# Optimization experiments

Measured on AMD Instinct MI355X. Metric: run time of the kernel, lower is better.

Reference implementation:

```python
import jax, jax.numpy as jnp
import numpy as np

NUM_CLASSES = 1000
TEMPERATURE = 0.1
B, B_OOD, D = 4096, 4096, 512


def _l2norm(x):
    return x / jnp.linalg.norm(x, axis=-1, keepdims=True)


def setup_inputs() -> dict:
    key = jax.random.key(0)
    k1, k2, k3, k4, k5 = jax.random.split(key, 5)
    return {
        "centers1": _l2norm(jax.random.normal(k1, (NUM_CLASSES, D), dtype=jnp.float32)),
        "features": _l2norm(jax.random.normal(k2, (B, D), dtype=jnp.float32)),
        "targets": jax.random.randint(k3, (B,), 0, NUM_CLASSES, dtype=jnp.int64 if jax.config.jax_enable_x64 else jnp.int32),
        "features_ood": _l2norm(jax.random.normal(k4, (B_OOD, D), dtype=jnp.float32)),
        "pseudo_target_ood": jax.random.randint(k5, (B_OOD,), 0, NUM_CLASSES, dtype=jnp.int64 if jax.config.jax_enable_x64 else jnp.int32),
    }


def reference(centers1, features, targets, features_ood, pseudo_target_ood):
    C = centers1.shape[0]
    b = features.shape[0]
    bo = features_ood.shape[0]
    n = b + C + bo  # total anchors: batch + class centers + ood

    centers_lbl = jnp.arange(C, dtype=targets.dtype)
    ood_lbl = jnp.full((bo,), C, dtype=targets.dtype)  # ood gets label == num_classes
    targets_all = jnp.concatenate([targets, centers_lbl, ood_lbl])              # [N]
    targets_all_class = jnp.concatenate([targets, centers_lbl, pseudo_target_ood])  # [N]

    # per-class count over all N labels (pseudo labels for ood)
    batch_cls_count = jnp.zeros((C,), dtype=jnp.float32).at[targets_all_class].add(1.0)

    # positive mask: same label as anchor, excluding self (diagonal for j < B)
    mask = (targets_all[:b, None] == targets_all[None, :]).astype(jnp.float32)  # [B,N]
    logits_mask = 1.0 - (jnp.arange(n)[None, :] == jnp.arange(b)[:, None]).astype(jnp.float32)
    mask = mask * logits_mask

    features_all = jnp.concatenate([features, centers1, features_ood], axis=0)  # [N,D]
    logits = jnp.matmul(features, features_all.T) / TEMPERATURE                 # [B,N]
    logits = logits - jax.lax.stop_gradient(jnp.max(logits, axis=1, keepdims=True))

    exp_logits = jnp.exp(logits) * logits_mask
    # class-balanced per-instance weight (count of the column's class, minus positive mask)
    per_ins_weight = batch_cls_count[targets_all_class][None, :] - mask         # [B,N]
    exp_logits_sum = jnp.sum(exp_logits / per_ins_weight, axis=1, keepdims=True)
    log_prob = logits - jnp.log(exp_logits_sum)

    mean_log_prob_pos = jnp.sum(mask * log_prob, axis=1) / jnp.sum(mask, axis=1)
    loss = -jnp.mean(mean_log_prob_pos)
    return loss
```

## Files before the change

### kernel.cpp

```cpp
#include <hip/hip_runtime.h>
#include <hip/hip_bf16.h>
#include <stdint.h>

#define NUM_C 1000
#define NB    4096
#define NO    4096
#define NCOL  9192
#define NPAD  9216
#define DK    512
#define BM    128
#define BN    256
#define BK    32
#define INV_T 10.0f

typedef __attribute__((ext_vector_type(8))) short short8;
typedef __attribute__((ext_vector_type(4))) float f32x4;

#define OFF_FALL 0u
#define OFF_CNT  9437184u
#define OFF_CNTT 9441280u
#define OFF_S    9445376u
#define OFF_P    9461760u
#define ZERO_BYTES 40960u

__device__ __forceinline__ void async16(const void* g, void* l) {
  __builtin_amdgcn_global_load_lds((const __attribute__((address_space(1))) void*)g,
                                   (__attribute__((address_space(3))) void*)l,
                                   16, 0, 0);
}

__device__ __forceinline__ ushort f2bf_rne(float f) {
  uint32_t u = __builtin_bit_cast(uint32_t, f);
  u += 0x7FFFu + ((u >> 16) & 1u);
  return (ushort)(u >> 16);
}

__global__ __launch_bounds__(256) void prep_k(const float* __restrict__ centers,
                                              const float* __restrict__ feats,
                                              const float* __restrict__ ood,
                                              const int* __restrict__ targets,
                                              const int* __restrict__ pseudo,
                                              ushort* __restrict__ fall,
                                              unsigned* __restrict__ cnt,
                                              unsigned* __restrict__ cntT) {
  int idx = blockIdx.x * 256 + threadIdx.x;
  int row = idx >> 6;
  int ck  = (idx & 63) * 8;
  ushort h[8];
  const float* src = nullptr;
  if (row < NB)              src = feats   + (size_t)row * DK + ck;
  else if (row < NB + NUM_C) src = centers + (size_t)(row - NB) * DK + ck;
  else if (row < NCOL)       src = ood     + (size_t)(row - NB - NUM_C) * DK + ck;
  if (src) {
    float4 v0 = *(const float4*)(src);
    float4 v1 = *(const float4*)(src + 4);
    h[0] = f2bf_rne(v0.x); h[1] = f2bf_rne(v0.y); h[2] = f2bf_rne(v0.z); h[3] = f2bf_rne(v0.w);
    h[4] = f2bf_rne(v1.x); h[5] = f2bf_rne(v1.y); h[6] = f2bf_rne(v1.z); h[7] = f2bf_rne(v1.w);
  } else {
    for (int i = 0; i < 8; i++) h[i] = 0;
  }
  *(uint4*)(fall + (size_t)row * DK + ck) = *(uint4*)h;

  if (blockIdx.x < 16) {
    int i = blockIdx.x * 256 + threadIdx.x;
    int t = targets[i];
    atomicAdd(&cnt[t], 1u);
    atomicAdd(&cntT[t], 1u);
    atomicAdd(&cnt[pseudo[i]], 1u);
  }
}

__global__ __launch_bounds__(256, 2) void gemm_fused(const ushort* __restrict__ fall,
                                                     const int* __restrict__ targets,
                                                     const int* __restrict__ pseudo,
                                                     const unsigned* __restrict__ cnt,
                                                     float* __restrict__ Sacc,
                                                     float* __restrict__ Pacc) {
  __shared__ ushort As[BM * BK];
  __shared__ ushort Bs[BN * BK];
  __shared__ int    sLbl[BN];
  __shared__ float  sRw0[BN];
  __shared__ float  sRw1[BN];
  __shared__ int    sTgt[BM];

  const int tid   = threadIdx.x;
  const int nTile = blockIdx.x;
  const int mTile = blockIdx.y;
  const int lane  = tid & 63;
  const int wv    = tid >> 6;
  const int wm    = wv >> 1;
  const int wn    = wv & 1;
  const int q     = lane >> 4;
  const int cIdx  = lane & 15;

  {
    int j = nTile * BN + tid;
    int lbl, tac;
    if (j >= NCOL)         { lbl = -1; tac = -1; }
    else if (j < NB)       { tac = targets[j]; lbl = tac; }
    else if (j < NB+NUM_C) { tac = j - NB;     lbl = tac; }
    else                   { tac = pseudo[j - NB - NUM_C]; lbl = NUM_C; }
    sLbl[tid] = lbl;
    if (tac >= 0) {
      float w = (float)(cnt[tac] + 1u);
      sRw0[tid] = 1.0f / w;
      sRw1[tid] = 1.0f / (w - 1.0f);
    } else {
      sRw0[tid] = 0.f;
      sRw1[tid] = 0.f;
    }
    if (tid < BM) sTgt[tid] = targets[mTile * BM + tid];
  }

  f32x4 acc[4][8];
#pragma unroll
  for (int mi = 0; mi < 4; mi++)
#pragma unroll
    for (int ni = 0; ni < 8; ni++)
      acc[mi][ni] = (f32x4){0.f, 0.f, 0.f, 0.f};

  const int aRow0 = mTile * BM;
  const int bRow0 = nTile * BN;
  const int sRow  = tid >> 2;
  const int sKo   = (tid & 3) * 8;

  for (int kt = 0; kt < DK; kt += BK) {
    __syncthreads();
    async16(fall + (size_t)(aRow0 + sRow)       * DK + kt + sKo, &As[sRow * BK + sKo]);
    async16(fall + (size_t)(aRow0 + 64 + sRow)  * DK + kt + sKo, &As[(64 + sRow) * BK + sKo]);
    async16(fall + (size_t)(bRow0 + sRow)       * DK + kt + sKo, &Bs[sRow * BK + sKo]);
    async16(fall + (size_t)(bRow0 + 64 + sRow)  * DK + kt + sKo, &Bs[(64 + sRow) * BK + sKo]);
    async16(fall + (size_t)(bRow0 + 128 + sRow) * DK + kt + sKo, &Bs[(128 + sRow) * BK + sKo]);
    async16(fall + (size_t)(bRow0 + 192 + sRow) * DK + kt + sKo, &Bs[(192 + sRow) * BK + sKo]);
    __syncthreads();

    short8 af[4], bfr[8];
#pragma unroll
    for (int mi = 0; mi < 4; mi++)
      af[mi] = *(const short8*)&As[(wm * 64 + mi * 16 + cIdx) * BK + q * 8];
#pragma unroll
    for (int ni = 0; ni < 8; ni++)
      bfr[ni] = *(const short8*)&Bs[(wn * 128 + ni * 16 + cIdx) * BK + q * 8];
#pragma unroll
    for (int mi = 0; mi < 4; mi++)
#pragma unroll
      for (int ni = 0; ni < 8; ni++)
        acc[mi][ni] = __builtin_amdgcn_mfma_f32_16x16x32_bf16(af[mi], bfr[ni], acc[mi][ni], 0, 0, 0);
  }

  float vS[16], vP[16];
#pragma unroll
  for (int s = 0; s < 16; s++) { vS[s] = 0.f; vP[s] = 0.f; }

#pragma unroll
  for (int ni = 0; ni < 8; ni++) {
    int jloc = wn * 128 + ni * 16 + cIdx;
    int j    = nTile * BN + jloc;
    int lblj = sLbl[jloc];
    float rw0 = sRw0[jloc], rw1 = sRw1[jloc];
#pragma unroll
    for (int mi = 0; mi < 4; mi++) {
      f32x4 a = acc[mi][ni];
#pragma unroll
      for (int r = 0; r < 4; r++) {
        int iloc = wm * 64 + mi * 16 + q * 4 + r;
        int i    = mTile * BM + iloc;
        int ti   = sTgt[iloc];
        float l  = a[r] * INV_T;
        bool diag = (j == i);
        bool pos  = (lblj == ti) && !diag;
        float rw  = diag ? 0.0f : (pos ? rw1 : rw0);
        float e   = __expf(l - 10.0f) * rw;
        vS[mi * 4 + r] += e;
        vP[mi * 4 + r] += pos ? l : 0.0f;
      }
    }
  }

#define RED_STEP(m, s, h)                                        \
  {                                                              \
    float sendS = (cIdx & (m)) ? vS[(s)] : vS[(s) + (h)];        \
    float sendP = (cIdx & (m)) ? vP[(s)] : vP[(s) + (h)];        \
    float rS = __shfl_xor(sendS, (m), 64);                       \
    float rP = __shfl_xor(sendP, (m), 64);                       \
    vS[(s)] = ((cIdx & (m)) ? vS[(s) + (h)] : vS[(s)]) + rS;     \
    vP[(s)] = ((cIdx & (m)) ? vP[(s) + (h)] : vP[(s)]) + rP;     \
  }
  RED_STEP(8, 0, 8) RED_STEP(8, 1, 8) RED_STEP(8, 2, 8) RED_STEP(8, 3, 8)
  RED_STEP(8, 4, 8) RED_STEP(8, 5, 8) RED_STEP(8, 6, 8) RED_STEP(8, 7, 8)
  RED_STEP(4, 0, 4) RED_STEP(4, 1, 4) RED_STEP(4, 2, 4) RED_STEP(4, 3, 4)
  RED_STEP(2, 0, 2) RED_STEP(2, 1, 2)
  RED_STEP(1, 0, 1)
#undef RED_STEP

  {
    int rowLoc = wm * 64 + (cIdx >> 2) * 16 + q * 4 + (cIdx & 3);
    int i = mTile * BM + rowLoc;
    atomicAdd(&Sacc[i], vS[0]);
    atomicAdd(&Pacc[i], vP[0]);
  }
}

__global__ __launch_bounds__(256) void finalize_k(const float* __restrict__ S,
                                                  const float* __restrict__ P,
                                                  const int* __restrict__ targets,
                                                  const unsigned* __restrict__ cntT,
                                                  float* __restrict__ out) {
  __shared__ float red[4];
  int tid = threadIdx.x;
  float local = 0.f;
  for (int i = tid; i < NB; i += 256) {
    float npos = (float)cntT[targets[i]];
    local += P[i] / npos - INV_T - __logf(S[i]);
  }
  for (int m = 1; m < 64; m <<= 1) local += __shfl_xor(local, m, 64);
  if ((tid & 63) == 0) red[tid >> 6] = local;
  __syncthreads();
  if (tid == 0) {
    float t = red[0] + red[1] + red[2] + red[3];
    out[0] = -t / (float)NB;
  }
}

extern "C" void kernel_launch(void* const* d_in, const int* in_sizes, int n_in,
                              void* d_out, int out_size, void* d_ws, size_t ws_size,
                              hipStream_t stream) {
  const float* centers = (const float*)d_in[0];
  const float* feats   = (const float*)d_in[1];
  const int*   targets = (const int*)d_in[2];
  const float* ood     = (const float*)d_in[3];
  const int*   pseudo  = (const int*)d_in[4];

  char* ws = (char*)d_ws;
  ushort*   fall = (ushort*)(ws + OFF_FALL);
  unsigned* cnt  = (unsigned*)(ws + OFF_CNT);
  unsigned* cntT = (unsigned*)(ws + OFF_CNTT);
  float*    Sacc = (float*)(ws + OFF_S);
  float*    Pacc = (float*)(ws + OFF_P);

  hipMemsetAsync(ws + OFF_CNT, 0, ZERO_BYTES, stream);
  prep_k<<<dim3((NPAD * 64) / 256), 256, 0, stream>>>(centers, feats, ood, targets, pseudo,
                                                      fall, cnt, cntT);
  gemm_fused<<<dim3(NPAD / BN, NB / BM), 256, 0, stream>>>(fall, targets, pseudo, cnt, Sacc, Pacc);
  finalize_k<<<1, 256, 0, stream>>>(Sacc, Pacc, targets, cntT, (float*)d_out);
}
```

Baseline: 144.0 us.

## Switch GEMM operands to FP8 e4m3 and replace memset with per-block histograms

Features are converted to FP8 e4m3 instead of bf16, and the GEMM uses the 16x16x32 fp8 MFMA, with a swizzled LDS layout and half as many async loads per K step. Class counts are built in shared-memory histograms per block and written as partials that the GEMM and finalize kernels sum. This drops the memset launch; the S/P accumulators are now zeroed inside prep_k. FP8 operands lower the precision of the logits, and since the temperature scales them by ten, rounding error in the exponentials grows and may hurt accuracy.

```diff
diff --git a/kernel.cpp b/kernel.cpp
--- a/kernel.cpp
+++ b/kernel.cpp
@@ -1,27 +1,23 @@
 #include <hip/hip_runtime.h>
-#include <hip/hip_bf16.h>
 #include <stdint.h>
 
 #define NUM_C 1000
 #define NB    4096
-#define NO    4096
 #define NCOL  9192
 #define NPAD  9216
 #define DK    512
 #define BM    128
 #define BN    256
-#define BK    32
+#define BKB   32
 #define INV_T 10.0f
 
-typedef __attribute__((ext_vector_type(8))) short short8;
 typedef __attribute__((ext_vector_type(4))) float f32x4;
 
-#define OFF_FALL 0u
-#define OFF_CNT  9437184u
-#define OFF_CNTT 9441280u
-#define OFF_S    9445376u
-#define OFF_P    9461760u
-#define ZERO_BYTES 40960u
+#define OFF_FALL  0u
+#define OFF_CNTP  4718592u
+#define OFF_CNTTP 4784128u
+#define OFF_S     4849664u
+#define OFF_P     4866048u
 
 __device__ __forceinline__ void async16(const void* g, void* l) {
   __builtin_amdgcn_global_load_lds((const __attribute__((address_space(1))) void*)g,
@@ -29,10 +25,32 @@
                                    16, 0, 0);
 }
 
-__device__ __forceinline__ ushort f2bf_rne(float f) {
-  uint32_t u = __builtin_bit_cast(uint32_t, f);
-  u += 0x7FFFu + ((u >> 16) & 1u);
-  return (ushort)(u >> 16);
+__device__ __forceinline__ unsigned sw_e4m3(float x) {
+  float ax = fabsf(x);
+  unsigned s = (__float_as_uint(x) >> 24) & 0x80u;
+  if (ax < 0.015625f) {
+    int n = (int)rintf(ax * 512.0f);
+    if (n >= 8) return s | 0x08u;
+    return s | (unsigned)n;
+  }
+  if (ax >= 448.0f) return s | 0x7Eu;
+  unsigned u = __float_as_uint(ax);
+  int ee = (int)(u >> 23) - 127;
+  float scale = __uint_as_float((unsigned)(3 - ee + 127) << 23);
+  int qv = (int)rintf(ax * scale);
+  if (qv == 16) { ee++; qv = 8; }
+  return s | (unsigned)(((ee + 7) << 3) | (qv - 8));
+}
+
+template <bool HI>
+__device__ __forceinline__ int cvt2(float a, float b, int old) {
+#if __has_builtin(__builtin_amdgcn_cvt_pk_fp8_f32)
+  return __builtin_amdgcn_cvt_pk_fp8_f32(a, b, old, HI);
+#else
+  unsigned pk = sw_e4m3(a) | (sw_e4m3(b) << 8);
+  return HI ? (int)(((unsigned)old & 0x0000FFFFu) | (pk << 16))
+            : (int)(((unsigned)old & 0xFFFF0000u) | pk);
+#endif
 }
 
 __global__ __launch_bounds__(256) void prep_k(const float* __restrict__ centers,
@@ -40,44 +58,60 @@
                                               const float* __restrict__ ood,
                                               const int* __restrict__ targets,
                                               const int* __restrict__ pseudo,
-                                              ushort* __restrict__ fall,
-                                              unsigned* __restrict__ cnt,
-                                              unsigned* __restrict__ cntT) {
-  int idx = blockIdx.x * 256 + threadIdx.x;
-  int row = idx >> 6;
-  int ck  = (idx & 63) * 8;
-  ushort h[8];
+                                              unsigned char* __restrict__ fall,
+                                              unsigned* __restrict__ cntP,
+                                              unsigned* __restrict__ cntTP,
+                                              float* __restrict__ SP) {
+  __shared__ unsigned hc[1024];
+  __shared__ unsigned hct[1024];
+  const int tid = threadIdx.x;
+
+  int idx = blockIdx.x * 256 + tid;
+  int row = idx >> 5;
+  int ck  = (idx & 31) * 16;
   const float* src = nullptr;
   if (row < NB)              src = feats   + (size_t)row * DK + ck;
   else if (row < NB + NUM_C) src = centers + (size_t)(row - NB) * DK + ck;
   else if (row < NCOL)       src = ood     + (size_t)(row - NB - NUM_C) * DK + ck;
+  unsigned w[4] = {0u, 0u, 0u, 0u};
   if (src) {
-    float4 v0 = *(const float4*)(src);
-    float4 v1 = *(const float4*)(src + 4);
-    h[0] = f2bf_rne(v0.x); h[1] = f2bf_rne(v0.y); h[2] = f2bf_rne(v0.z); h[3] = f2bf_rne(v0.w);
-    h[4] = f2bf_rne(v1.x); h[5] = f2bf_rne(v1.y); h[6] = f2bf_rne(v1.z); h[7] = f2bf_rne(v1.w);
-  } else {
-    for (int i = 0; i < 8; i++) h[i] = 0;
-  }
-  *(uint4*)(fall + (size_t)row * DK + ck) = *(uint4*)h;
+#pragma unroll
+    for (int g = 0; g < 4; g++) {
+      float4 v0 = *(const float4*)(src + g * 4);
+      int p = 0;
+      p = cvt2<false>(v0.x, v0.y, p);
+      p = cvt2<true>(v0.z, v0.w, p);
+      w[g] = (unsigned)p;
+    }
+  }
+  *(uint4*)(fall + (size_t)row * DK + ck) = make_uint4(w[0], w[1], w[2], w[3]);
 
   if (blockIdx.x < 16) {
-    int i = blockIdx.x * 256 + threadIdx.x;
+    for (int k = tid; k < 1024; k += 256) { hc[k] = 0u; hct[k] = 0u; }
+    __syncthreads();
+    int i = blockIdx.x * 256 + tid;
     int t = targets[i];
-    atomicAdd(&cnt[t], 1u);
-    atomicAdd(&cntT[t], 1u);
-    atomicAdd(&cnt[pseudo[i]], 1u);
-  }
-}
-
-__global__ __launch_bounds__(256, 2) void gemm_fused(const ushort* __restrict__ fall,
+    atomicAdd(&hc[t], 1u);
+    atomicAdd(&hct[t], 1u);
+    atomicAdd(&hc[pseudo[i]], 1u);
+    __syncthreads();
+    for (int k = tid; k < 1024; k += 256) {
+      cntP[blockIdx.x * 1024 + k]  = hc[k];
+      cntTP[blockIdx.x * 1024 + k] = hct[k];
+    }
+  } else if (blockIdx.x < 48) {
+    SP[(blockIdx.x - 16) * 256 + tid] = 0.0f;
+  }
+}
+
+__global__ __launch_bounds__(256, 2) void gemm_fused(const unsigned char* __restrict__ fall,
                                                      const int* __restrict__ targets,
                                                      const int* __restrict__ pseudo,
-                                                     const unsigned* __restrict__ cnt,
+                                                     const unsigned* __restrict__ cntP,
                                                      float* __restrict__ Sacc,
                                                      float* __restrict__ Pacc) {
-  __shared__ ushort As[BM * BK];
-  __shared__ ushort Bs[BN * BK];
+  __shared__ unsigned char As[BM * BKB];
+  __shared__ unsigned char Bs[BN * BKB];
   __shared__ int    sLbl[BN];
   __shared__ float  sRw0[BN];
   __shared__ float  sRw1[BN];
@@ -102,7 +136,10 @@
     else                   { tac = pseudo[j - NB - NUM_C]; lbl = NUM_C; }
     sLbl[tid] = lbl;
     if (tac >= 0) {
-      float w = (float)(cnt[tac] + 1u);
+      unsigned c = 1u;
+#pragma unroll
+      for (int b = 0; b < 16; b++) c += cntP[b * 1024 + tac];
+      float w = (float)c;
       sRw0[tid] = 1.0f / w;
       sRw1[tid] = 1.0f / (w - 1.0f);
     } else {
@@ -121,31 +158,38 @@
 
   const int aRow0 = mTile * BM;
   const int bRow0 = nTile * BN;
-  const int sRow  = tid >> 2;
-  const int sKo   = (tid & 3) * 8;
-
-  for (int kt = 0; kt < DK; kt += BK) {
-    __syncthreads();
-    async16(fall + (size_t)(aRow0 + sRow)       * DK + kt + sKo, &As[sRow * BK + sKo]);
-    async16(fall + (size_t)(aRow0 + 64 + sRow)  * DK + kt + sKo, &As[(64 + sRow) * BK + sKo]);
-    async16(fall + (size_t)(bRow0 + sRow)       * DK + kt + sKo, &Bs[sRow * BK + sKo]);
-    async16(fall + (size_t)(bRow0 + 64 + sRow)  * DK + kt + sKo, &Bs[(64 + sRow) * BK + sKo]);
-    async16(fall + (size_t)(bRow0 + 128 + sRow) * DK + kt + sKo, &Bs[(128 + sRow) * BK + sKo]);
-    async16(fall + (size_t)(bRow0 + 192 + sRow) * DK + kt + sKo, &Bs[(192 + sRow) * BK + sKo]);
-    __syncthreads();
-
-    short8 af[4], bfr[8];
+
+  const int sRow = tid >> 1;
+  const int cg   = (tid & 1) ^ (sRow & 1);
+  const unsigned char* gA  = fall + (size_t)(aRow0 + sRow)       * DK + cg * 16;
+  const unsigned char* gB0 = fall + (size_t)(bRow0 + sRow)       * DK + cg * 16;
+  const unsigned char* gB1 = fall + (size_t)(bRow0 + 128 + sRow) * DK + cg * 16;
+  unsigned char* lA  = As + tid * 16;
+  unsigned char* lB0 = Bs + tid * 16;
+  unsigned char* lB1 = Bs + 4096 + tid * 16;
+
+  const int fOff = ((((q >> 1) ^ (cIdx & 1)) << 4) | ((q & 1) << 3));
+
+  for (int kt = 0; kt < DK; kt += BKB) {
+    __syncthreads();
+    async16(gA + kt, lA);
+    async16(gB0 + kt, lB0);
+    async16(gB1 + kt, lB1);
+    __syncthreads();
+
+    long long af[4];
+    long long bf8[8];
 #pragma unroll
     for (int mi = 0; mi < 4; mi++)
-      af[mi] = *(const short8*)&As[(wm * 64 + mi * 16 + cIdx) * BK + q * 8];
+      af[mi] = *(const long long*)&As[(wm * 64 + mi * 16 + cIdx) * BKB + fOff];
 #pragma unroll
     for (int ni = 0; ni < 8; ni++)
-      bfr[ni] = *(const short8*)&Bs[(wn * 128 + ni * 16 + cIdx) * BK + q * 8];
+      bf8[ni] = *(const long long*)&Bs[(wn * 128 + ni * 16 + cIdx) * BKB + fOff];
 #pragma unroll
     for (int mi = 0; mi < 4; mi++)
 #pragma unroll
       for (int ni = 0; ni < 8; ni++)
-        acc[mi][ni] = __builtin_amdgcn_mfma_f32_16x16x32_bf16(af[mi], bfr[ni], acc[mi][ni], 0, 0, 0);
+        acc[mi][ni] = __builtin_amdgcn_mfma_f32_16x16x32_fp8_fp8(af[mi], bf8[ni], acc[mi][ni], 0, 0, 0);
   }
 
   float vS[16], vP[16];
@@ -204,13 +248,21 @@
 __global__ __launch_bounds__(256) void finalize_k(const float* __restrict__ S,
                                                   const float* __restrict__ P,
                                                   const int* __restrict__ targets,
-                                                  const unsigned* __restrict__ cntT,
+                                                  const unsigned* __restrict__ cntTP,
                                                   float* __restrict__ out) {
+  __shared__ unsigned ct[1024];
   __shared__ float red[4];
   int tid = threadIdx.x;
+  for (int k = tid; k < 1024; k += 256) {
+    unsigned c = 0u;
+#pragma unroll
+    for (int b = 0; b < 16; b++) c += cntTP[b * 1024 + k];
+    ct[k] = c;
+  }
+  __syncthreads();
   float local = 0.f;
   for (int i = tid; i < NB; i += 256) {
-    float npos = (float)cntT[targets[i]];
+    float npos = (float)ct[targets[i]];
     local += P[i] / npos - INV_T - __logf(S[i]);
   }
   for (int m = 1; m < 64; m <<= 1) local += __shfl_xor(local, m, 64);
@@ -232,15 +284,14 @@
   const int*   pseudo  = (const int*)d_in[4];
 
   char* ws = (char*)d_ws;
-  ushort*   fall = (ushort*)(ws + OFF_FALL);
-  unsigned* cnt  = (unsigned*)(ws + OFF_CNT);
-  unsigned* cntT = (unsigned*)(ws + OFF_CNTT);
-  float*    Sacc = (float*)(ws + OFF_S);
-  float*    Pacc = (float*)(ws + OFF_P);
-
-  hipMemsetAsync(ws + OFF_CNT, 0, ZERO_BYTES, stream);
-  prep_k<<<dim3((NPAD * 64) / 256), 256, 0, stream>>>(centers, feats, ood, targets, pseudo,
-                                                      fall, cnt, cntT);
-  gemm_fused<<<dim3(NPAD / BN, NB / BM), 256, 0, stream>>>(fall, targets, pseudo, cnt, Sacc, Pacc);
-  finalize_k<<<1, 256, 0, stream>>>(Sacc, Pacc, targets, cntT, (float*)d_out);
-}
+  unsigned char* fall  = (unsigned char*)(ws + OFF_FALL);
+  unsigned*      cntP  = (unsigned*)(ws + OFF_CNTP);
+  unsigned*      cntTP = (unsigned*)(ws + OFF_CNTTP);
+  float*         Sacc  = (float*)(ws + OFF_S);
+  float*         Pacc  = (float*)(ws + OFF_P);
+
+  prep_k<<<dim3((NPAD * 32) / 256), 256, 0, stream>>>(centers, feats, ood, targets, pseudo,
+                                                      fall, cntP, cntTP, Sacc);
+  gemm_fused<<<dim3(NPAD / BN, NB / BM), 256, 0, stream>>>(fall, targets, pseudo, cntP, Sacc, Pacc);
+  finalize_k<<<1, 256, 0, stream>>>(Sacc, Pacc, targets, cntTP, (float*)d_out);
+}
```

Result: slower. 147.4 us (+2.3%).
